# Performance work log

Measured on AMD Instinct MI355X. Metric: run time of the kernel, lower is better.

Reference implementation:

```python
import jax, jax.numpy as jnp
import numpy as np

D_OUT = 10          # number of classes (d_out)
TEMP = 1.0          # temperature T
EPS = 1e-07         # log eps from original code


def setup_inputs() -> dict:
    key = jax.random.key(0)
    k1, k2, k3, k4, k5 = jax.random.split(key, 5)
    N, M, d_in, dim = 2048, 131072, 128, 128
    x = jax.random.normal(k1, (N, d_in), dtype=jnp.float32)
    candidate_x = jax.random.normal(k2, (M, d_in), dtype=jnp.float32)
    candidate_y = jax.random.randint(k3, (M,), 0, D_OUT)
    # encoder = nn.Linear(d_in, dim): weight [dim, d_in], bias [dim]
    W = jax.random.normal(k4, (dim, d_in), dtype=jnp.float32) / np.float32(np.sqrt(d_in))
    b = jax.random.normal(k5, (dim,), dtype=jnp.float32) * 0.01
    return {"x": x, "candidate_x": candidate_x, "candidate_y": candidate_y, "W": W, "b": b}


def reference(x, candidate_x, candidate_y, W, b):
    # encoder (mode=0, n_blocks=0): single linear layer
    z = x @ W.T + b                 # [N, dim]
    zc = candidate_x @ W.T + b      # [M, dim]
    # torch.cdist(z, zc, p=2): pairwise euclidean distances [N, M]
    sq = (jnp.sum(z * z, axis=-1, keepdims=True)
          + jnp.sum(zc * zc, axis=-1)[None, :]
          - 2.0 * (z @ zc.T))
    dist = jnp.sqrt(jnp.maximum(sq, 1e-12)) / TEMP
    # is_train=False: no diagonal masking, no candidate subsampling
    probs = jax.nn.softmax(-dist, axis=-1)            # [N, M]
    onehot = jax.nn.one_hot(candidate_y, D_OUT, dtype=z.dtype)  # [M, D_OUT]
    logits = probs @ onehot                           # [N, D_OUT]
    return jnp.log(logits + EPS)
```

## Files before the change

### kernel.cpp

```cpp
#include <hip/hip_runtime.h>
#include <stdint.h>
#include <math.h>

#define N_ROWS 2048
#define M_CAND 131072
#define DIMK 128
#define DOUT 10
#define COLS_PER_BLOCK 1024
#define SUB_ITERS 16
#define CHUNKS_MAX 138
#define M_PAD_MAX (CHUNKS_MAX * COLS_PER_BLOCK)
#define LOG2E 1.4426950408889634f
#define L2E2 (LOG2E * LOG2E)

typedef __attribute__((ext_vector_type(8))) __bf16 bf16x8;
typedef __attribute__((ext_vector_type(8))) short s16x8;
typedef __attribute__((ext_vector_type(4))) float f32x4;
typedef __attribute__((ext_vector_type(2))) float f32x2;
typedef __attribute__((address_space(3))) void lds_void;
typedef const __attribute__((address_space(1))) void gbl_void;

union frag_cast { s16x8 s; bf16x8 b; };

__device__ __forceinline__ short f2bf(float f) {
  union { float f; unsigned u; } v; v.f = f;
  return (short)((v.u + 0x7fffu + ((v.u >> 16) & 1u)) >> 16);
}
__device__ __forceinline__ float bf2f(short h) {
  union { unsigned u; float f; } v;
  v.u = ((unsigned)(unsigned short)h) << 16; return v.f;
}
__device__ __forceinline__ float fast_sqrtf(float x) {
#if __has_builtin(__builtin_amdgcn_sqrtf)
  return __builtin_amdgcn_sqrtf(x);
#else
  return sqrtf(x);
#endif
}
__device__ __forceinline__ float fast_exp2f(float x) {
#if __has_builtin(__builtin_amdgcn_exp2f)
  return __builtin_amdgcn_exp2f(x);
#else
  return exp2f(x);
#endif
}

__device__ __forceinline__ void stage64(const short* gbase, short* lds, int t) {
  int w = t >> 6;
#pragma unroll
  for (int i = 0; i < 4; ++i) {
    int flat = i * 256 + t;
    int r = flat >> 4, s = flat & 15;
    int g = s ^ (r & 15);
    const short* src = gbase + r * DIMK + g * 8;
    short* dst = lds + (i * 256 + w * 64) * 8;
    __builtin_amdgcn_global_load_lds((gbl_void*)src, (lds_void*)dst, 16, 0, 0);
  }
}

__device__ __forceinline__ void stage128(const short* gbase, short* lds, int t) {
  int w = t >> 6;
#pragma unroll
  for (int i = 0; i < 8; ++i) {
    int flat = i * 256 + t;
    int r = flat >> 4, s = flat & 15;
    int g = s ^ (r & 15);
    const short* src = gbase + r * DIMK + g * 8;
    short* dst = lds + (i * 256 + w * 64) * 8;
    __builtin_amdgcn_global_load_lds((gbl_void*)src, (lds_void*)dst, 16, 0, 0);
  }
}

__global__ __launch_bounds__(256) void hist_kernel(const int* __restrict__ y,
                                                   int* __restrict__ cnt) {
  __shared__ int h[DOUT];
  int t = threadIdx.x;
  if (t < DOUT) h[t] = 0;
  __syncthreads();
  atomicAdd(&h[y[blockIdx.x * 256 + t]], 1);
  __syncthreads();
  if (t < DOUT) cnt[blockIdx.x * DOUT + t] = h[t];
}

__global__ __launch_bounds__(512) void scan_kernel(const int* __restrict__ cnt,
                                                   int* __restrict__ blockoff,
                                                   int* __restrict__ chunk_class,
                                                   int* __restrict__ invperm) {
  __shared__ int buf[2][512 * DOUT];
  __shared__ int pbnd[DOUT + 1];
  __shared__ int ccnt[DOUT];
  int t = threadIdx.x;
  int v[DOUT];
#pragma unroll
  for (int c = 0; c < DOUT; ++c) { v[c] = cnt[t * DOUT + c]; buf[0][t * DOUT + c] = v[c]; }
  __syncthreads();
  int src = 0;
  for (int off = 1; off < 512; off <<= 1) {
    int x[DOUT];
#pragma unroll
    for (int c = 0; c < DOUT; ++c) {
      x[c] = buf[src][t * DOUT + c];
      if (t >= off) x[c] += buf[src][(t - off) * DOUT + c];
    }
#pragma unroll
    for (int c = 0; c < DOUT; ++c) buf[1 - src][t * DOUT + c] = x[c];
    src ^= 1;
    __syncthreads();
  }
  if (t == 0) {
    int pb = 0;
    pbnd[0] = 0;
    for (int c = 0; c < DOUT; ++c) {
      int tot = buf[src][511 * DOUT + c];
      ccnt[c] = tot;
      pb += (tot + COLS_PER_BLOCK - 1) & ~(COLS_PER_BLOCK - 1);
      pbnd[c + 1] = pb;
    }
  }
  __syncthreads();
  if (t < CHUNKS_MAX) {
    int col = t * COLS_PER_BLOCK, c = 0;
#pragma unroll
    for (int k = 1; k < DOUT; ++k) c += (col >= pbnd[k]) ? 1 : 0;
    chunk_class[t] = c;
  }
  for (int c = 0; c < DOUT; ++c)
    for (int i = pbnd[c] + ccnt[c] + t; i < pbnd[c + 1]; i += 512) invperm[i] = -1;
  for (int i = pbnd[DOUT] + t; i < M_PAD_MAX; i += 512) invperm[i] = -1;
#pragma unroll
  for (int c = 0; c < DOUT; ++c)
    blockoff[t * DOUT + c] = pbnd[c] + buf[src][t * DOUT + c] - v[c];
}

__global__ __launch_bounds__(256) void scatter_kernel(const int* __restrict__ y,
                                                      const int* __restrict__ blockoff,
                                                      int* __restrict__ invperm) {
  __shared__ int cur[DOUT];
  int t = threadIdx.x;
  if (t < DOUT) cur[t] = blockoff[blockIdx.x * DOUT + t];
  __syncthreads();
  int e = blockIdx.x * 256 + t;
  int p = atomicAdd(&cur[y[e]], 1);
  invperm[p] = e;
}

__global__ __launch_bounds__(256) void convert_w_kernel(const float* __restrict__ W,
                                                        short* __restrict__ Wb) {
  int i = blockIdx.x * 256 + threadIdx.x;
  Wb[i] = f2bf(W[i]);
}

__global__ __launch_bounds__(256, 4) void encoder2_kernel(
    const float* __restrict__ X, const short* __restrict__ Wb,
    const float* __restrict__ bias, const int* __restrict__ invperm,
    short* __restrict__ Zb, float* __restrict__ Sq) {
  __shared__ __align__(16) short Ws[DIMK * DIMK];
  int t = threadIdx.x;
  int lane = t & 63, wid = t >> 6;
  int quad = lane >> 4, l15 = lane & 15;
  int rowbase = blockIdx.x * 64 + wid * 16;

  stage128(Wb, Ws, t);

  int grow = rowbase + l15;
  int gxr = invperm ? invperm[grow] : grow;
  bool dead = (gxr < 0);

  bf16x8 afrag[4];
#pragma unroll
  for (int ks = 0; ks < 4; ++ks) {
    frag_cast fc;
    if (!dead) {
      const float* p = X + (size_t)gxr * DIMK + ks * 32 + quad * 8;
      float4 x0 = *(const float4*)p;
      float4 x1 = *(const float4*)(p + 4);
      fc.s[0] = f2bf(x0.x); fc.s[1] = f2bf(x0.y); fc.s[2] = f2bf(x0.z); fc.s[3] = f2bf(x0.w);
      fc.s[4] = f2bf(x1.x); fc.s[5] = f2bf(x1.y); fc.s[6] = f2bf(x1.z); fc.s[7] = f2bf(x1.w);
    } else {
      fc.s = (s16x8){0, 0, 0, 0, 0, 0, 0, 0};
    }
    afrag[ks] = fc.b;
  }

  float bias_v[8];
#pragma unroll
  for (int j = 0; j < 8; ++j) bias_v[j] = bias[j * 16 + l15];

  __syncthreads();

  f32x4 acc[8];
#pragma unroll
  for (int j = 0; j < 8; ++j) acc[j] = (f32x4){0.f, 0.f, 0.f, 0.f};

#pragma unroll
  for (int ks = 0; ks < 4; ++ks) {
    int slot = (ks * 4 + quad) ^ l15;
    const short* p = Ws + l15 * DIMK + slot * 8;
#pragma unroll
    for (int j = 0; j < 8; ++j) {
      bf16x8 b = *(const bf16x8*)(p + j * 16 * DIMK);
      acc[j] = __builtin_amdgcn_mfma_f32_16x16x32_bf16(afrag[ks], b, acc[j], 0, 0, 0);
    }
  }

  float sqp[4] = {0.f, 0.f, 0.f, 0.f};
#pragma unroll
  for (int j = 0; j < 8; ++j) {
#pragma unroll
    for (int r = 0; r < 4; ++r) {
      float z = acc[j][r] + bias_v[j];
      short hb = f2bf(z);
      float zr = bf2f(hb);
      sqp[r] = fmaf(zr, zr, sqp[r]);
      Zb[(size_t)(rowbase + quad * 4 + r) * DIMK + j * 16 + l15] = hb;
    }
  }
#pragma unroll
  for (int r = 0; r < 4; ++r) {
    float s = sqp[r];
    s += __shfl_xor(s, 1);
    s += __shfl_xor(s, 2);
    s += __shfl_xor(s, 4);
    s += __shfl_xor(s, 8);
    if (l15 == 0) {
      int row = rowbase + quad * 4 + r;
      bool drow = invperm && (invperm[row] < 0);
      Sq[row] = drow ? 1e30f : s * L2E2;
    }
  }
}

__global__ __launch_bounds__(256, 4) void nca_main(
    const short* __restrict__ Zb, const short* __restrict__ Cb,
    const float* __restrict__ Sqz, const float* __restrict__ Sqc,
    float* __restrict__ partials) {
  __shared__ __align__(16) short Bs[2][64 * DIMK];

  int t = threadIdx.x;
  int lane = t & 63, wid = t >> 6;
  int quad = lane >> 4, l15 = lane & 15;
  int wrow = wid * 32;
  int rowbase = blockIdx.x * 128;
  int colbase0 = blockIdx.y * COLS_PER_BLOCK;

  stage64(Cb + (size_t)colbase0 * DIMK, &Bs[0][0], t);

  bf16x8 afrag[4][2];
#pragma unroll
  for (int ks = 0; ks < 4; ++ks)
#pragma unroll
    for (int ti = 0; ti < 2; ++ti)
      afrag[ks][ti] = *(const bf16x8*)(
          Zb + (size_t)(rowbase + wrow + ti * 16 + l15) * DIMK + ks * 32 + quad * 8);

  f32x2 szv2[2][2];
#pragma unroll
  for (int ti = 0; ti < 2; ++ti) {
    f32x4 s4 = *(const f32x4*)(Sqz + rowbase + wrow + ti * 16 + quad * 4);
    szv2[ti][0] = (f32x2){s4[0], s4[1]};
    szv2[ti][1] = (f32x2){s4[2], s4[3]};
  }

  f32x2 sum2[4];
#pragma unroll
  for (int i = 0; i < 4; ++i) sum2[i] = (f32x2){0.f, 0.f};

  const f32x2 m2 = {-2.0f * L2E2, -2.0f * L2E2};

  for (int it = 0; it < SUB_ITERS; ++it) {
    int colb = colbase0 + it * 64;
    __syncthreads();

    float sqcv[4];
#pragma unroll
    for (int j = 0; j < 4; ++j) sqcv[j] = Sqc[colb + j * 16 + l15];

    if (it + 1 < SUB_ITERS)
      stage64(Cb + (size_t)(colb + 64) * DIMK, &Bs[(it + 1) & 1][0], t);
    const short* B = &Bs[it & 1][0];

    f32x4 acc[2][4];
    f32x4 z4 = {0.f, 0.f, 0.f, 0.f};
#pragma unroll
    for (int ti = 0; ti < 2; ++ti)
#pragma unroll
      for (int j = 0; j < 4; ++j) acc[ti][j] = z4;

#pragma unroll
    for (int ks = 0; ks < 4; ++ks) {
      int slot = (ks * 4 + quad) ^ l15;
      const short* p = B + l15 * DIMK + slot * 8;
      bf16x8 b0 = *(const bf16x8*)(p);
      bf16x8 b1 = *(const bf16x8*)(p + 16 * DIMK);
      bf16x8 b2 = *(const bf16x8*)(p + 32 * DIMK);
      bf16x8 b3 = *(const bf16x8*)(p + 48 * DIMK);
#pragma unroll
      for (int ti = 0; ti < 2; ++ti) {
        acc[ti][0] = __builtin_amdgcn_mfma_f32_16x16x32_bf16(afrag[ks][ti], b0, acc[ti][0], 0, 0, 0);
        acc[ti][1] = __builtin_amdgcn_mfma_f32_16x16x32_bf16(afrag[ks][ti], b1, acc[ti][1], 0, 0, 0);
        acc[ti][2] = __builtin_amdgcn_mfma_f32_16x16x32_bf16(afrag[ks][ti], b2, acc[ti][2], 0, 0, 0);
        acc[ti][3] = __builtin_amdgcn_mfma_f32_16x16x32_bf16(afrag[ks][ti], b3, acc[ti][3], 0, 0, 0);
      }
    }

#pragma unroll
    for (int ti = 0; ti < 2; ++ti)
#pragma unroll
      for (int j = 0; j < 4; ++j) {
        f32x2 q = {sqcv[j], sqcv[j]};
        f32x2 s01 = szv2[ti][0] + q;
        f32x2 s23 = szv2[ti][1] + q;
        f32x4 a = acc[ti][j];
        f32x2 a01 = {a[0], a[1]}, a23 = {a[2], a[3]};
        s01 = a01 * m2 + s01;
        s23 = a23 * m2 + s23;
        float e0 = fast_exp2f(-fast_sqrtf(__builtin_fabsf(s01[0])));
        float e1 = fast_exp2f(-fast_sqrtf(__builtin_fabsf(s01[1])));
        float e2 = fast_exp2f(-fast_sqrtf(__builtin_fabsf(s23[0])));
        float e3 = fast_exp2f(-fast_sqrtf(__builtin_fabsf(s23[1])));
        sum2[ti * 2 + 0] += (f32x2){e0, e1};
        sum2[ti * 2 + 1] += (f32x2){e2, e3};
      }
  }

#pragma unroll
  for (int si = 0; si < 8; ++si) {
    float s = sum2[si >> 1][si & 1];
    s += __shfl_xor(s, 1);
    s += __shfl_xor(s, 2);
    s += __shfl_xor(s, 4);
    s += __shfl_xor(s, 8);
    if (l15 == 0) {
      int row_l = wrow + (si >> 2) * 16 + quad * 4 + (si & 3);
      partials[(size_t)blockIdx.y * N_ROWS + rowbase + row_l] = s;
    }
  }
}

__global__ __launch_bounds__(64) void reduce_kernel(const float* __restrict__ partials,
                                                    const int* __restrict__ chunk_class,
                                                    float* __restrict__ out) {
  int row = blockIdx.x, lane = threadIdx.x;
  float s = 0.f;
  for (int ch = 0; ch < CHUNKS_MAX; ++ch) {
    float p = partials[(size_t)ch * N_ROWS + row];
    int c = chunk_class[ch];
    s += (lane == c) ? p : 0.f;
  }
  float tot = s;
  tot += __shfl_xor(tot, 1);
  tot += __shfl_xor(tot, 2);
  tot += __shfl_xor(tot, 4);
  tot += __shfl_xor(tot, 8);
  tot += __shfl_xor(tot, 16);
  tot += __shfl_xor(tot, 32);
  if (lane < DOUT)
    out[(size_t)row * DOUT + lane] = logf(s / tot + 1e-7f);
}

extern "C" void kernel_launch(void* const* d_in, const int* in_sizes, int n_in,
                              void* d_out, int out_size, void* d_ws, size_t ws_size,
                              hipStream_t stream) {
  const float* x = (const float*)d_in[0];
  const float* cx = (const float*)d_in[1];
  const int* cy = (const int*)d_in[2];
  const float* W = (const float*)d_in[3];
  const float* bias = (const float*)d_in[4];
  float* out = (float*)d_out;
  char* ws = (char*)d_ws;

  size_t off = 0;
  auto alloc = [&](size_t bytes) {
    void* p = ws + off;
    off = (off + bytes + 255) & ~(size_t)255;
    return p;
  };
  short* Zb = (short*)alloc((size_t)N_ROWS * DIMK * 2);
  short* Cb = (short*)alloc((size_t)M_PAD_MAX * DIMK * 2);
  short* Wb = (short*)alloc((size_t)DIMK * DIMK * 2);
  float* Sqz = (float*)alloc((size_t)N_ROWS * 4);
  float* Sqc = (float*)alloc((size_t)M_PAD_MAX * 4);
  int* invperm = (int*)alloc((size_t)M_PAD_MAX * 4);
  int* cnt = (int*)alloc(512 * DOUT * 4);
  int* blockoff = (int*)alloc(512 * DOUT * 4);
  int* chunk_class = (int*)alloc(CHUNKS_MAX * 4);
  float* partials = (float*)alloc((size_t)CHUNKS_MAX * N_ROWS * 4);
  if (off > ws_size) return;

  hist_kernel<<<M_CAND / 256, 256, 0, stream>>>(cy, cnt);
  scan_kernel<<<1, 512, 0, stream>>>(cnt, blockoff, chunk_class, invperm);
  scatter_kernel<<<M_CAND / 256, 256, 0, stream>>>(cy, blockoff, invperm);
  convert_w_kernel<<<DIMK * DIMK / 256, 256, 0, stream>>>(W, Wb);
  encoder2_kernel<<<N_ROWS / 64, 256, 0, stream>>>(x, Wb, bias, nullptr, Zb, Sqz);
  encoder2_kernel<<<M_PAD_MAX / 64, 256, 0, stream>>>(cx, Wb, bias, invperm, Cb, Sqc);
  nca_main<<<dim3(N_ROWS / 128, CHUNKS_MAX), 256, 0, stream>>>(Zb, Cb, Sqz, Sqc, partials);
  reduce_kernel<<<N_ROWS, 64, 0, stream>>>(partials, chunk_class, out);
}
```

Measured before the change: 246.1 us.

## Pad classes to 64 columns with variable-length chunks instead of 1024

Candidate columns grouped by class are now padded only to multiples of 64 rather than 1024. Each chunk records its start and number of 64-column sub-tiles, and empty chunks exit early. This removes most of the padded dummy columns that nca_main used to process. The encoder now writes through a forward permutation (scatter store) instead of gathering through an inverse permutation, and the W conversion is fused into the histogram kernel to drop one launch. The cost is scattered output writes from the encoder and variable loop trip counts in the main kernel.

```diff
diff --git a/kernel.cpp b/kernel.cpp
--- a/kernel.cpp
+++ b/kernel.cpp
@@ -6,10 +6,10 @@
 #define M_CAND 131072
 #define DIMK 128
 #define DOUT 10
-#define COLS_PER_BLOCK 1024
-#define SUB_ITERS 16
+#define SUB_COLS 64
+#define MAX_SUB 16
 #define CHUNKS_MAX 138
-#define M_PAD_MAX (CHUNKS_MAX * COLS_PER_BLOCK)
+#define M_ALLOC (M_CAND + 1024)
 #define LOG2E 1.4426950408889634f
 #define L2E2 (LOG2E * LOG2E)
 
@@ -72,22 +72,28 @@
 }
 
 __global__ __launch_bounds__(256) void hist_kernel(const int* __restrict__ y,
-                                                   int* __restrict__ cnt) {
+                                                   int* __restrict__ cnt,
+                                                   const float* __restrict__ W,
+                                                   short* __restrict__ Wb) {
   __shared__ int h[DOUT];
   int t = threadIdx.x;
+  int gi = blockIdx.x * 256 + t;
+  if (gi < DIMK * DIMK) Wb[gi] = f2bf(W[gi]);
   if (t < DOUT) h[t] = 0;
   __syncthreads();
-  atomicAdd(&h[y[blockIdx.x * 256 + t]], 1);
+  atomicAdd(&h[y[gi]], 1);
   __syncthreads();
   if (t < DOUT) cnt[blockIdx.x * DOUT + t] = h[t];
 }
 
 __global__ __launch_bounds__(512) void scan_kernel(const int* __restrict__ cnt,
                                                    int* __restrict__ blockoff,
+                                                   int* __restrict__ chunk_start,
+                                                   int* __restrict__ chunk_nsub,
                                                    int* __restrict__ chunk_class,
-                                                   int* __restrict__ invperm) {
+                                                   float* __restrict__ Sqc) {
   __shared__ int buf[2][512 * DOUT];
-  __shared__ int pbnd[DOUT + 1];
+  __shared__ int cstart[DOUT];
   __shared__ int ccnt[DOUT];
   int t = threadIdx.x;
   int v[DOUT];
@@ -109,50 +115,52 @@
   }
   if (t == 0) {
     int pb = 0;
-    pbnd[0] = 0;
     for (int c = 0; c < DOUT; ++c) {
       int tot = buf[src][511 * DOUT + c];
       ccnt[c] = tot;
-      pb += (tot + COLS_PER_BLOCK - 1) & ~(COLS_PER_BLOCK - 1);
-      pbnd[c + 1] = pb;
-    }
-  }
-  __syncthreads();
-  if (t < CHUNKS_MAX) {
-    int col = t * COLS_PER_BLOCK, c = 0;
-#pragma unroll
-    for (int k = 1; k < DOUT; ++k) c += (col >= pbnd[k]) ? 1 : 0;
-    chunk_class[t] = c;
-  }
+      cstart[c] = pb;
+      pb += (tot + 63) & ~63;
+    }
+    int idx = 0;
+    for (int c = 0; c < DOUT; ++c) {
+      int c64 = (ccnt[c] + 63) & ~63;
+      for (int i = 0; i * 1024 < c64; ++i) {
+        int rem = (c64 - i * 1024) / SUB_COLS;
+        chunk_start[idx] = cstart[c] + i * 1024;
+        chunk_nsub[idx] = rem < MAX_SUB ? rem : MAX_SUB;
+        chunk_class[idx] = c;
+        ++idx;
+      }
+    }
+    for (; idx < CHUNKS_MAX; ++idx) {
+      chunk_start[idx] = 0; chunk_nsub[idx] = 0; chunk_class[idx] = DOUT - 1;
+    }
+  }
+  __syncthreads();
+  for (int c = 0; c < DOUT; ++c) {
+    int b = cstart[c] + ccnt[c], e = cstart[c] + ((ccnt[c] + 63) & ~63);
+    for (int i = b + t; i < e; i += 512) Sqc[i] = 1e30f;
+  }
+#pragma unroll
   for (int c = 0; c < DOUT; ++c)
-    for (int i = pbnd[c] + ccnt[c] + t; i < pbnd[c + 1]; i += 512) invperm[i] = -1;
-  for (int i = pbnd[DOUT] + t; i < M_PAD_MAX; i += 512) invperm[i] = -1;
-#pragma unroll
-  for (int c = 0; c < DOUT; ++c)
-    blockoff[t * DOUT + c] = pbnd[c] + buf[src][t * DOUT + c] - v[c];
+    blockoff[t * DOUT + c] = cstart[c] + buf[src][t * DOUT + c] - v[c];
 }
 
 __global__ __launch_bounds__(256) void scatter_kernel(const int* __restrict__ y,
                                                       const int* __restrict__ blockoff,
-                                                      int* __restrict__ invperm) {
+                                                      int* __restrict__ perm) {
   __shared__ int cur[DOUT];
   int t = threadIdx.x;
   if (t < DOUT) cur[t] = blockoff[blockIdx.x * DOUT + t];
   __syncthreads();
   int e = blockIdx.x * 256 + t;
   int p = atomicAdd(&cur[y[e]], 1);
-  invperm[p] = e;
-}
-
-__global__ __launch_bounds__(256) void convert_w_kernel(const float* __restrict__ W,
-                                                        short* __restrict__ Wb) {
-  int i = blockIdx.x * 256 + threadIdx.x;
-  Wb[i] = f2bf(W[i]);
+  perm[e] = p;
 }
 
 __global__ __launch_bounds__(256, 4) void encoder2_kernel(
     const float* __restrict__ X, const short* __restrict__ Wb,
-    const float* __restrict__ bias, const int* __restrict__ invperm,
+    const float* __restrict__ bias, const int* __restrict__ perm,
     short* __restrict__ Zb, float* __restrict__ Sq) {
   __shared__ __align__(16) short Ws[DIMK * DIMK];
   int t = threadIdx.x;
@@ -162,29 +170,28 @@
 
   stage128(Wb, Ws, t);
 
-  int grow = rowbase + l15;
-  int gxr = invperm ? invperm[grow] : grow;
-  bool dead = (gxr < 0);
-
   bf16x8 afrag[4];
 #pragma unroll
   for (int ks = 0; ks < 4; ++ks) {
     frag_cast fc;
-    if (!dead) {
-      const float* p = X + (size_t)gxr * DIMK + ks * 32 + quad * 8;
-      float4 x0 = *(const float4*)p;
-      float4 x1 = *(const float4*)(p + 4);
-      fc.s[0] = f2bf(x0.x); fc.s[1] = f2bf(x0.y); fc.s[2] = f2bf(x0.z); fc.s[3] = f2bf(x0.w);
-      fc.s[4] = f2bf(x1.x); fc.s[5] = f2bf(x1.y); fc.s[6] = f2bf(x1.z); fc.s[7] = f2bf(x1.w);
-    } else {
-      fc.s = (s16x8){0, 0, 0, 0, 0, 0, 0, 0};
-    }
+    const float* p = X + (size_t)(rowbase + l15) * DIMK + ks * 32 + quad * 8;
+    float4 x0 = *(const float4*)p;
+    float4 x1 = *(const float4*)(p + 4);
+    fc.s[0] = f2bf(x0.x); fc.s[1] = f2bf(x0.y); fc.s[2] = f2bf(x0.z); fc.s[3] = f2bf(x0.w);
+    fc.s[4] = f2bf(x1.x); fc.s[5] = f2bf(x1.y); fc.s[6] = f2bf(x1.z); fc.s[7] = f2bf(x1.w);
     afrag[ks] = fc.b;
   }
 
   float bias_v[8];
 #pragma unroll
   for (int j = 0; j < 8; ++j) bias_v[j] = bias[j * 16 + l15];
+
+  int orow[4];
+#pragma unroll
+  for (int r = 0; r < 4; ++r) {
+    int rr = rowbase + quad * 4 + r;
+    orow[r] = perm ? perm[rr] : rr;
+  }
 
   __syncthreads();
 
@@ -212,7 +219,7 @@
       short hb = f2bf(z);
       float zr = bf2f(hb);
       sqp[r] = fmaf(zr, zr, sqp[r]);
-      Zb[(size_t)(rowbase + quad * 4 + r) * DIMK + j * 16 + l15] = hb;
+      Zb[(size_t)orow[r] * DIMK + j * 16 + l15] = hb;
     }
   }
 #pragma unroll
@@ -222,28 +229,32 @@
     s += __shfl_xor(s, 2);
     s += __shfl_xor(s, 4);
     s += __shfl_xor(s, 8);
-    if (l15 == 0) {
-      int row = rowbase + quad * 4 + r;
-      bool drow = invperm && (invperm[row] < 0);
-      Sq[row] = drow ? 1e30f : s * L2E2;
-    }
+    if (l15 == 0) Sq[orow[r]] = s * L2E2;
   }
 }
 
 __global__ __launch_bounds__(256, 4) void nca_main(
     const short* __restrict__ Zb, const short* __restrict__ Cb,
     const float* __restrict__ Sqz, const float* __restrict__ Sqc,
+    const int* __restrict__ chunk_start, const int* __restrict__ chunk_nsub,
     float* __restrict__ partials) {
   __shared__ __align__(16) short Bs[2][64 * DIMK];
 
   int t = threadIdx.x;
+  int cidx = blockIdx.y;
+  int rowbase = blockIdx.x * 128;
+  int nsub = chunk_nsub[cidx];
+  if (nsub == 0) {
+    if (t < 128) partials[(size_t)cidx * N_ROWS + rowbase + t] = 0.f;
+    return;
+  }
+  int start = chunk_start[cidx];
+
   int lane = t & 63, wid = t >> 6;
   int quad = lane >> 4, l15 = lane & 15;
   int wrow = wid * 32;
-  int rowbase = blockIdx.x * 128;
-  int colbase0 = blockIdx.y * COLS_PER_BLOCK;
-
-  stage64(Cb + (size_t)colbase0 * DIMK, &Bs[0][0], t);
+
+  stage64(Cb + (size_t)start * DIMK, &Bs[0][0], t);
 
   bf16x8 afrag[4][2];
 #pragma unroll
@@ -267,15 +278,15 @@
 
   const f32x2 m2 = {-2.0f * L2E2, -2.0f * L2E2};
 
-  for (int it = 0; it < SUB_ITERS; ++it) {
-    int colb = colbase0 + it * 64;
+  for (int it = 0; it < nsub; ++it) {
+    int colb = start + it * 64;
     __syncthreads();
 
     float sqcv[4];
 #pragma unroll
     for (int j = 0; j < 4; ++j) sqcv[j] = Sqc[colb + j * 16 + l15];
 
-    if (it + 1 < SUB_ITERS)
+    if (it + 1 < nsub)
       stage64(Cb + (size_t)(colb + 64) * DIMK, &Bs[(it + 1) & 1][0], t);
     const short* B = &Bs[it & 1][0];
 
@@ -332,7 +343,7 @@
     s += __shfl_xor(s, 8);
     if (l15 == 0) {
       int row_l = wrow + (si >> 2) * 16 + quad * 4 + (si & 3);
-      partials[(size_t)blockIdx.y * N_ROWS + rowbase + row_l] = s;
+      partials[(size_t)cidx * N_ROWS + rowbase + row_l] = s;
     }
   }
 }
@@ -376,23 +387,26 @@
     return p;
   };
   short* Zb = (short*)alloc((size_t)N_ROWS * DIMK * 2);
-  short* Cb = (short*)alloc((size_t)M_PAD_MAX * DIMK * 2);
+  short* Cb = (short*)alloc((size_t)M_ALLOC * DIMK * 2);
   short* Wb = (short*)alloc((size_t)DIMK * DIMK * 2);
   float* Sqz = (float*)alloc((size_t)N_ROWS * 4);
-  float* Sqc = (float*)alloc((size_t)M_PAD_MAX * 4);
-  int* invperm = (int*)alloc((size_t)M_PAD_MAX * 4);
+  float* Sqc = (float*)alloc((size_t)M_ALLOC * 4);
+  int* perm = (int*)alloc((size_t)M_CAND * 4);
   int* cnt = (int*)alloc(512 * DOUT * 4);
   int* blockoff = (int*)alloc(512 * DOUT * 4);
+  int* chunk_start = (int*)alloc(CHUNKS_MAX * 4);
+  int* chunk_nsub = (int*)alloc(CHUNKS_MAX * 4);
   int* chunk_class = (int*)alloc(CHUNKS_MAX * 4);
   float* partials = (float*)alloc((size_t)CHUNKS_MAX * N_ROWS * 4);
   if (off > ws_size) return;
 
-  hist_kernel<<<M_CAND / 256, 256, 0, stream>>>(cy, cnt);
-  scan_kernel<<<1, 512, 0, stream>>>(cnt, blockoff, chunk_class, invperm);
-  scatter_kernel<<<M_CAND / 256, 256, 0, stream>>>(cy, blockoff, invperm);
-  convert_w_kernel<<<DIMK * DIMK / 256, 256, 0, stream>>>(W, Wb);
+  hist_kernel<<<M_CAND / 256, 256, 0, stream>>>(cy, cnt, W, Wb);
+  scan_kernel<<<1, 512, 0, stream>>>(cnt, blockoff, chunk_start, chunk_nsub,
+                                     chunk_class, Sqc);
+  scatter_kernel<<<M_CAND / 256, 256, 0, stream>>>(cy, blockoff, perm);
   encoder2_kernel<<<N_ROWS / 64, 256, 0, stream>>>(x, Wb, bias, nullptr, Zb, Sqz);
-  encoder2_kernel<<<M_PAD_MAX / 64, 256, 0, stream>>>(cx, Wb, bias, invperm, Cb, Sqc);
-  nca_main<<<dim3(N_ROWS / 128, CHUNKS_MAX), 256, 0, stream>>>(Zb, Cb, Sqz, Sqc, partials);
+  encoder2_kernel<<<M_CAND / 64, 256, 0, stream>>>(cx, Wb, bias, perm, Cb, Sqc);
+  nca_main<<<dim3(N_ROWS / 128, CHUNKS_MAX), 256, 0, stream>>>(
+      Zb, Cb, Sqz, Sqc, chunk_start, chunk_nsub, partials);
   reduce_kernel<<<N_ROWS, 64, 0, stream>>>(partials, chunk_class, out);
 }
```

New measurement: 251.9 us. +2.4%, slower.

## Replace gather-based candidate permutation with atomic scatter and fuse preprocessing kernels

Applied to the files above, without the earlier changes.

Folds the W bf16 conversion into the histogram kernel and replaces the block-level prefix scan with a single-block atomic class total and per-class global cursors. Candidates are scattered by their own thread through an atomic slot index instead of gathered via an inverse permutation. Both encoder launches are merged into one grid that writes outputs to permuted rows with nontemporal stores. This cuts launch count and the serial scan, at the cost of nondeterministic ordering within a class and padding rows in Cb that are no longer zeroed, relying only on a sentinel norm.

```diff
diff --git a/kernel.cpp b/kernel.cpp
--- a/kernel.cpp
+++ b/kernel.cpp
@@ -10,6 +10,7 @@
 #define SUB_ITERS 16
 #define CHUNKS_MAX 138
 #define M_PAD_MAX (CHUNKS_MAX * COLS_PER_BLOCK)
+#define NBLK_X (N_ROWS / 64)
 #define LOG2E 1.4426950408889634f
 #define L2E2 (LOG2E * LOG2E)
 
@@ -72,48 +73,43 @@
 }
 
 __global__ __launch_bounds__(256) void hist_kernel(const int* __restrict__ y,
-                                                   int* __restrict__ cnt) {
+                                                   int* __restrict__ cnt,
+                                                   const float* __restrict__ W,
+                                                   short* __restrict__ Wb) {
   __shared__ int h[DOUT];
   int t = threadIdx.x;
+  int gi = blockIdx.x * 256 + t;
+  if (gi < DIMK * DIMK) Wb[gi] = f2bf(W[gi]);
   if (t < DOUT) h[t] = 0;
   __syncthreads();
-  atomicAdd(&h[y[blockIdx.x * 256 + t]], 1);
+  atomicAdd(&h[y[gi]], 1);
   __syncthreads();
   if (t < DOUT) cnt[blockIdx.x * DOUT + t] = h[t];
 }
 
-__global__ __launch_bounds__(512) void scan_kernel(const int* __restrict__ cnt,
-                                                   int* __restrict__ blockoff,
-                                                   int* __restrict__ chunk_class,
-                                                   int* __restrict__ invperm) {
-  __shared__ int buf[2][512 * DOUT];
+__global__ __launch_bounds__(512) void setup_kernel(const int* __restrict__ cnt,
+                                                    int* __restrict__ cursor,
+                                                    int* __restrict__ chunk_class,
+                                                    float* __restrict__ Sqc) {
+  __shared__ int h[DOUT];
   __shared__ int pbnd[DOUT + 1];
   __shared__ int ccnt[DOUT];
   int t = threadIdx.x;
+  if (t < DOUT) h[t] = 0;
+  __syncthreads();
   int v[DOUT];
 #pragma unroll
-  for (int c = 0; c < DOUT; ++c) { v[c] = cnt[t * DOUT + c]; buf[0][t * DOUT + c] = v[c]; }
-  __syncthreads();
-  int src = 0;
-  for (int off = 1; off < 512; off <<= 1) {
-    int x[DOUT];
-#pragma unroll
-    for (int c = 0; c < DOUT; ++c) {
-      x[c] = buf[src][t * DOUT + c];
-      if (t >= off) x[c] += buf[src][(t - off) * DOUT + c];
-    }
-#pragma unroll
-    for (int c = 0; c < DOUT; ++c) buf[1 - src][t * DOUT + c] = x[c];
-    src ^= 1;
-    __syncthreads();
-  }
+  for (int c = 0; c < DOUT; ++c) v[c] = cnt[t * DOUT + c];
+#pragma unroll
+  for (int c = 0; c < DOUT; ++c) atomicAdd(&h[c], v[c]);
+  __syncthreads();
   if (t == 0) {
     int pb = 0;
     pbnd[0] = 0;
     for (int c = 0; c < DOUT; ++c) {
-      int tot = buf[src][511 * DOUT + c];
-      ccnt[c] = tot;
-      pb += (tot + COLS_PER_BLOCK - 1) & ~(COLS_PER_BLOCK - 1);
+      ccnt[c] = h[c];
+      cursor[c] = pb;
+      pb += (h[c] + COLS_PER_BLOCK - 1) & ~(COLS_PER_BLOCK - 1);
       pbnd[c + 1] = pb;
     }
   }
@@ -124,67 +120,60 @@
     for (int k = 1; k < DOUT; ++k) c += (col >= pbnd[k]) ? 1 : 0;
     chunk_class[t] = c;
   }
-  for (int c = 0; c < DOUT; ++c)
-    for (int i = pbnd[c] + ccnt[c] + t; i < pbnd[c + 1]; i += 512) invperm[i] = -1;
-  for (int i = pbnd[DOUT] + t; i < M_PAD_MAX; i += 512) invperm[i] = -1;
-#pragma unroll
-  for (int c = 0; c < DOUT; ++c)
-    blockoff[t * DOUT + c] = pbnd[c] + buf[src][t * DOUT + c] - v[c];
+  for (int c = 0; c < DOUT; ++c) {
+    int b = pbnd[c] + ccnt[c], e = pbnd[c + 1];
+    for (int i = b + t; i < e; i += 512) Sqc[i] = 1e30f;
+  }
+  for (int i = pbnd[DOUT] + t; i < M_PAD_MAX; i += 512) Sqc[i] = 1e30f;
 }
 
 __global__ __launch_bounds__(256) void scatter_kernel(const int* __restrict__ y,
-                                                      const int* __restrict__ blockoff,
-                                                      int* __restrict__ invperm) {
-  __shared__ int cur[DOUT];
-  int t = threadIdx.x;
-  if (t < DOUT) cur[t] = blockoff[blockIdx.x * DOUT + t];
-  __syncthreads();
-  int e = blockIdx.x * 256 + t;
-  int p = atomicAdd(&cur[y[e]], 1);
-  invperm[p] = e;
-}
-
-__global__ __launch_bounds__(256) void convert_w_kernel(const float* __restrict__ W,
-                                                        short* __restrict__ Wb) {
-  int i = blockIdx.x * 256 + threadIdx.x;
-  Wb[i] = f2bf(W[i]);
-}
-
-__global__ __launch_bounds__(256, 4) void encoder2_kernel(
-    const float* __restrict__ X, const short* __restrict__ Wb,
-    const float* __restrict__ bias, const int* __restrict__ invperm,
-    short* __restrict__ Zb, float* __restrict__ Sq) {
+                                                      int* __restrict__ cursor,
+                                                      int* __restrict__ perm) {
+  int e = blockIdx.x * 256 + threadIdx.x;
+  perm[e] = atomicAdd(&cursor[y[e]], 1);
+}
+
+__global__ __launch_bounds__(256, 4) void encoder_kernel(
+    const float* __restrict__ X, const float* __restrict__ CX,
+    const short* __restrict__ Wb, const float* __restrict__ bias,
+    const int* __restrict__ perm,
+    short* __restrict__ Zb, short* __restrict__ Cb,
+    float* __restrict__ Sqz, float* __restrict__ Sqc) {
   __shared__ __align__(16) short Ws[DIMK * DIMK];
   int t = threadIdx.x;
   int lane = t & 63, wid = t >> 6;
   int quad = lane >> 4, l15 = lane & 15;
-  int rowbase = blockIdx.x * 64 + wid * 16;
+  bool is_x = blockIdx.x < NBLK_X;
+  int rowbase = (is_x ? blockIdx.x : blockIdx.x - NBLK_X) * 64 + wid * 16;
+  const float* src = is_x ? X : CX;
+  short* outZ = is_x ? Zb : Cb;
+  float* outS = is_x ? Sqz : Sqc;
 
   stage128(Wb, Ws, t);
-
-  int grow = rowbase + l15;
-  int gxr = invperm ? invperm[grow] : grow;
-  bool dead = (gxr < 0);
 
   bf16x8 afrag[4];
 #pragma unroll
   for (int ks = 0; ks < 4; ++ks) {
     frag_cast fc;
-    if (!dead) {
-      const float* p = X + (size_t)gxr * DIMK + ks * 32 + quad * 8;
-      float4 x0 = *(const float4*)p;
-      float4 x1 = *(const float4*)(p + 4);
-      fc.s[0] = f2bf(x0.x); fc.s[1] = f2bf(x0.y); fc.s[2] = f2bf(x0.z); fc.s[3] = f2bf(x0.w);
-      fc.s[4] = f2bf(x1.x); fc.s[5] = f2bf(x1.y); fc.s[6] = f2bf(x1.z); fc.s[7] = f2bf(x1.w);
-    } else {
-      fc.s = (s16x8){0, 0, 0, 0, 0, 0, 0, 0};
-    }
+    const float* p = src + (size_t)(rowbase + l15) * DIMK + ks * 32 + quad * 8;
+    float4 x0 = *(const float4*)p;
+    float4 x1 = *(const float4*)(p + 4);
+    fc.s[0] = f2bf(x0.x); fc.s[1] = f2bf(x0.y); fc.s[2] = f2bf(x0.z); fc.s[3] = f2bf(x0.w);
+    fc.s[4] = f2bf(x1.x); fc.s[5] = f2bf(x1.y); fc.s[6] = f2bf(x1.z); fc.s[7] = f2bf(x1.w);
     afrag[ks] = fc.b;
   }
 
   float bias_v[8];
 #pragma unroll
   for (int j = 0; j < 8; ++j) bias_v[j] = bias[j * 16 + l15];
+
+  int orow[4];
+#pragma unroll
+  for (int r = 0; r < 4; ++r) {
+    int rr = rowbase + quad * 4 + r;
+    orow[r] = is_x ? rr : perm[rr];
+  }
 
   __syncthreads();
 
@@ -212,7 +201,7 @@
       short hb = f2bf(z);
       float zr = bf2f(hb);
       sqp[r] = fmaf(zr, zr, sqp[r]);
-      Zb[(size_t)(rowbase + quad * 4 + r) * DIMK + j * 16 + l15] = hb;
+      __builtin_nontemporal_store(hb, &outZ[(size_t)orow[r] * DIMK + j * 16 + l15]);
     }
   }
 #pragma unroll
@@ -222,11 +211,8 @@
     s += __shfl_xor(s, 2);
     s += __shfl_xor(s, 4);
     s += __shfl_xor(s, 8);
-    if (l15 == 0) {
-      int row = rowbase + quad * 4 + r;
-      bool drow = invperm && (invperm[row] < 0);
-      Sq[row] = drow ? 1e30f : s * L2E2;
-    }
+    if (l15 == 0)
+      __builtin_nontemporal_store(s * L2E2, &outS[orow[r]]);
   }
 }
 
@@ -380,19 +366,19 @@
   short* Wb = (short*)alloc((size_t)DIMK * DIMK * 2);
   float* Sqz = (float*)alloc((size_t)N_ROWS * 4);
   float* Sqc = (float*)alloc((size_t)M_PAD_MAX * 4);
-  int* invperm = (int*)alloc((size_t)M_PAD_MAX * 4);
+  int* perm = (int*)alloc((size_t)M_CAND * 4);
   int* cnt = (int*)alloc(512 * DOUT * 4);
-  int* blockoff = (int*)alloc(512 * DOUT * 4);
+  int* cursor = (int*)alloc(16 * 4);
   int* chunk_class = (int*)alloc(CHUNKS_MAX * 4);
   float* partials = (float*)alloc((size_t)CHUNKS_MAX * N_ROWS * 4);
   if (off > ws_size) return;
 
-  hist_kernel<<<M_CAND / 256, 256, 0, stream>>>(cy, cnt);
-  scan_kernel<<<1, 512, 0, stream>>>(cnt, blockoff, chunk_class, invperm);
-  scatter_kernel<<<M_CAND / 256, 256, 0, stream>>>(cy, blockoff, invperm);
-  convert_w_kernel<<<DIMK * DIMK / 256, 256, 0, stream>>>(W, Wb);
-  encoder2_kernel<<<N_ROWS / 64, 256, 0, stream>>>(x, Wb, bias, nullptr, Zb, Sqz);
-  encoder2_kernel<<<M_PAD_MAX / 64, 256, 0, stream>>>(cx, Wb, bias, invperm, Cb, Sqc);
-  nca_main<<<dim3(N_ROWS / 128, CHUNKS_MAX), 256, 0, stream>>>(Zb, Cb, Sqz, Sqc, partials);
+  hist_kernel<<<M_CAND / 256, 256, 0, stream>>>(cy, cnt, W, Wb);
+  setup_kernel<<<1, 512, 0, stream>>>(cnt, cursor, chunk_class, Sqc);
+  scatter_kernel<<<M_CAND / 256, 256, 0, stream>>>(cy, cursor, perm);
+  encoder_kernel<<<NBLK_X + M_CAND / 64, 256, 0, stream>>>(
+      x, cx, Wb, bias, perm, Zb, Cb, Sqz, Sqc);
+  nca_main<<<dim3(N_ROWS / 128, CHUNKS_MAX), 256, 0, stream>>>(
+      Zb, Cb, Sqz, Sqc, partials);
   reduce_kernel<<<N_ROWS, 64, 0, stream>>>(partials, chunk_class, out);
 }
```

After: 695.4 us. +182.6%, slower.
